# Kernel optimization log

Measured on AMD Instinct MI355X. Metric: run time of the kernel, lower is better.

The kernel has to match this reference:

```python
import jax, jax.numpy as jnp
import numpy as np

B, SEQ_LEN, N_VARS, N_MARK = 16, 96, 862, 4
D_MODEL, D_STATE, D_CONV, D_FF = 512, 16, 2, 512
DT_RANK = 32  # ceil(d_model/16)
E_LAYERS = 2
PRED_LEN = 96
EPS = 1e-5


def _layer_norm(x, w, b):
    mu = x.mean(-1, keepdims=True)
    var = ((x - mu) ** 2).mean(-1, keepdims=True)
    return (x - mu) / jnp.sqrt(var + EPS) * w + b


def _selective_scan(xc, dt, Bm, Cm, A, D):
    # xc, dt: [B,S,d]; Bm, Cm: [B,S,ds]; A: [d,ds]; D: [d]
    def step(h, inp):
        x_t, dt_t, B_t, C_t = inp  # [B,d],[B,d],[B,ds],[B,ds]
        dA = jnp.exp(dt_t[..., None] * A)                      # [B,d,ds]
        h = dA * h + (dt_t * x_t)[..., None] * B_t[:, None, :]
        return h, jnp.einsum('bds,bs->bd', h, C_t)
    h0 = jnp.zeros((xc.shape[0], A.shape[0], A.shape[1]), xc.dtype)
    xs = tuple(jnp.swapaxes(t, 0, 1) for t in (xc, dt, Bm, Cm))
    _, ys = jax.lax.scan(step, h0, xs)
    return jnp.swapaxes(ys, 0, 1) + xc * D


def _mamba(x, in_W, conv_W, conv_b, xproj_W, dt_W, dt_b, A_log, D, out_W):
    d = in_W.shape[0] // 2
    xz = x @ in_W.T                                             # [B,S,2d]
    xi, z = xz[..., :d], xz[..., d:]
    xp = jnp.pad(xi, ((0, 0), (1, 0), (0, 0)))                  # causal pad, d_conv=2
    xc = xp[:, :-1] * conv_W[:, 0] + xp[:, 1:] * conv_W[:, 1] + conv_b
    xc = jax.nn.silu(xc)
    dbc = xc @ xproj_W.T                                        # [B,S,dt_rank+2*ds]
    dtr = dbc[..., :DT_RANK]
    Bm = dbc[..., DT_RANK:DT_RANK + D_STATE]
    Cm = dbc[..., DT_RANK + D_STATE:]
    dt = jax.nn.softplus(dtr @ dt_W.T + dt_b)
    A = -jnp.exp(A_log)
    y = _selective_scan(xc, dt, Bm, Cm, A, D)
    return (y * jax.nn.silu(z)) @ out_W.T


def _forward(x_enc, x_mark_enc, emb_W, emb_b,
             mf_in_W, mf_conv_W, mf_conv_b, mf_xproj_W, mf_dt_W, mf_dt_b, mf_A_log, mf_D, mf_out_W,
             mr_in_W, mr_conv_W, mr_conv_b, mr_xproj_W, mr_dt_W, mr_dt_b, mr_A_log, mr_D, mr_out_W,
             conv1_W, conv1_b, conv2_W, conv2_b, ln1_w, ln1_b, ln2_w, ln2_b,
             enc_norm_w, enc_norm_b, proj_W, proj_b):
    # RevIN-style instance normalization over time
    means = x_enc.mean(1, keepdims=True)
    xe = x_enc - means
    stdev = jnp.sqrt(jnp.mean(xe ** 2, axis=1, keepdims=True) + EPS)  # unbiased=False
    xe = xe / stdev
    N = x_enc.shape[2]
    # inverted embedding: variates (+ time marks) are tokens, Linear over time axis
    tok = jnp.concatenate([jnp.swapaxes(xe, 1, 2), jnp.swapaxes(x_mark_enc, 1, 2)], axis=1)
    x = tok @ emb_W.T + emb_b                                   # [B, N+4, d_model]
    for l in range(E_LAYERS):
        fwd = _mamba(x, mf_in_W[l], mf_conv_W[l], mf_conv_b[l], mf_xproj_W[l],
                     mf_dt_W[l], mf_dt_b[l], mf_A_log[l], mf_D[l], mf_out_W[l])
        rev = _mamba(x[:, ::-1], mr_in_W[l], mr_conv_W[l], mr_conv_b[l], mr_xproj_W[l],
                     mr_dt_W[l], mr_dt_b[l], mr_A_log[l], mr_D[l], mr_out_W[l])[:, ::-1]
        x = x + fwd + rev
        y = x = _layer_norm(x, ln1_w[l], ln1_b[l])
        y = jax.nn.relu(y @ conv1_W[l].T + conv1_b[l])          # 1x1 conv == linear
        y = y @ conv2_W[l].T + conv2_b[l]
        x = _layer_norm(x + y, ln2_w[l], ln2_b[l])
    x = _layer_norm(x, enc_norm_w, enc_norm_b)
    dec = jnp.swapaxes(x @ proj_W.T + proj_b, 1, 2)[:, :, :N]   # [B, pred_len, N]
    dec = dec * stdev[:, 0][:, None, :] + means[:, 0][:, None, :]
    return dec


def setup_inputs() -> dict:
    key = jax.random.key(0)
    ks = iter(jax.random.split(key, 64))
    nrm = lambda shape, s=0.02: jax.random.normal(next(ks), shape, jnp.float32) * s
    inp = {
        'x_enc': jax.random.normal(next(ks), (B, SEQ_LEN, N_VARS), jnp.float32),
        'x_mark_enc': jax.random.normal(next(ks), (B, SEQ_LEN, N_MARK), jnp.float32),
        'x_dec': jnp.zeros((1, 1, 1), jnp.float32),
        'x_mark_dec': jnp.zeros((1, 1, 1), jnp.float32),
        'emb_W': nrm((D_MODEL, SEQ_LEN)),
        'emb_b': jnp.zeros((D_MODEL,), jnp.float32),
    }
    for p in ('mf', 'mr'):
        inp[p + '_in_W'] = nrm((E_LAYERS, 2 * D_MODEL, D_MODEL))
        inp[p + '_conv_W'] = nrm((E_LAYERS, D_MODEL, D_CONV), 0.1)
        inp[p + '_conv_b'] = jnp.zeros((E_LAYERS, D_MODEL), jnp.float32)
        inp[p + '_xproj_W'] = nrm((E_LAYERS, DT_RANK + 2 * D_STATE, D_MODEL))
        inp[p + '_dt_W'] = nrm((E_LAYERS, D_MODEL, DT_RANK), 0.1)
        inp[p + '_dt_b'] = nrm((E_LAYERS, D_MODEL), 0.1)
        inp[p + '_A_log'] = jnp.log(jnp.broadcast_to(
            jnp.arange(1, D_STATE + 1, dtype=jnp.float32), (E_LAYERS, D_MODEL, D_STATE)))
        inp[p + '_D'] = jnp.ones((E_LAYERS, D_MODEL), jnp.float32)
        inp[p + '_out_W'] = nrm((E_LAYERS, D_MODEL, D_MODEL))
    inp['conv1_W'] = nrm((E_LAYERS, D_FF, D_MODEL))
    inp['conv1_b'] = jnp.zeros((E_LAYERS, D_FF), jnp.float32)
    inp['conv2_W'] = nrm((E_LAYERS, D_MODEL, D_FF))
    inp['conv2_b'] = jnp.zeros((E_LAYERS, D_MODEL), jnp.float32)
    inp['ln1_w'] = jnp.ones((E_LAYERS, D_MODEL), jnp.float32)
    inp['ln1_b'] = jnp.zeros((E_LAYERS, D_MODEL), jnp.float32)
    inp['ln2_w'] = jnp.ones((E_LAYERS, D_MODEL), jnp.float32)
    inp['ln2_b'] = jnp.zeros((E_LAYERS, D_MODEL), jnp.float32)
    inp['enc_norm_w'] = jnp.ones((D_MODEL,), jnp.float32)
    inp['enc_norm_b'] = jnp.zeros((D_MODEL,), jnp.float32)
    inp['proj_W'] = nrm((PRED_LEN, D_MODEL))
    inp['proj_b'] = jnp.zeros((PRED_LEN,), jnp.float32)
    return inp


def reference(x_enc, x_mark_enc, x_dec, x_mark_dec, emb_W, emb_b,
              mf_in_W, mf_conv_W, mf_conv_b, mf_xproj_W, mf_dt_W, mf_dt_b, mf_A_log, mf_D, mf_out_W,
              mr_in_W, mr_conv_W, mr_conv_b, mr_xproj_W, mr_dt_W, mr_dt_b, mr_A_log, mr_D, mr_out_W,
              conv1_W, conv1_b, conv2_W, conv2_b, ln1_w, ln1_b, ln2_w, ln2_b,
              enc_norm_w, enc_norm_b, proj_W, proj_b):
    return _forward(x_enc, x_mark_enc, emb_W, emb_b,
                    mf_in_W, mf_conv_W, mf_conv_b, mf_xproj_W, mf_dt_W, mf_dt_b, mf_A_log, mf_D, mf_out_W,
                    mr_in_W, mr_conv_W, mr_conv_b, mr_xproj_W, mr_dt_W, mr_dt_b, mr_A_log, mr_D, mr_out_W,
                    conv1_W, conv1_b, conv2_W, conv2_b, ln1_w, ln1_b, ln2_w, ln2_b,
                    enc_norm_w, enc_norm_b, proj_W, proj_b)
```

## Files before the change

kernel.cpp:

```cpp
#include <hip/hip_runtime.h>
#include <math.h>

#define BATCH   16
#define SEQ     96
#define NVARS   862
#define NMARK   4
#define LTOK    866
#define MROWS   (BATCH*LTOK)
#define DM      512
#define DSTATE  16
#define DTRANK  32
#define DFF     512
#define PRED    96
#define EPS_F   1e-5f

#define CCH     32
#define TCH     28

typedef __attribute__((ext_vector_type(4))) float f32x4;
typedef __attribute__((ext_vector_type(8))) short bf16x8;
typedef unsigned short ushort_t;

__device__ __forceinline__ short f2bf(float f) {
    unsigned u = __builtin_bit_cast(unsigned, f);
    u += 0x7fffu + ((u >> 16) & 1u);
    return (short)(u >> 16);
}
__device__ __forceinline__ float bf2f(ushort_t u) {
    return __builtin_bit_cast(float, (unsigned)u << 16);
}

__global__ __launch_bounds__(256) void gemm_bf16(
    const ushort_t* __restrict__ A, int lda,
    const ushort_t* __restrict__ W, int ldw,
    const float* __restrict__ bias,
    const float* __restrict__ res,
    float* __restrict__ out, int ldo,
    int M, int N, int K, int rev, int act, int final_mode, int gx,
    const float* __restrict__ fstd, const float* __restrict__ fmean)
{
    __shared__ ushort_t Als[128 * 32];
    __shared__ ushort_t Bls[128 * 32];
    const int tid  = threadIdx.x;
    const int lane = tid & 63;
    const int w    = tid >> 6;
    const int wm   = w >> 1;
    const int wn   = w & 1;

    const int nwg = gridDim.x;
    const int orig = blockIdx.x;
    const int q = nwg >> 3, r = nwg & 7;
    const int xcd = orig & 7, idx = orig >> 3;
    const int swz = (xcd < r ? xcd * (q + 1) : r * (q + 1) + (xcd - r) * q) + idx;
    const int m0 = (swz / gx) * 128, n0 = (swz % gx) * 128;

    const int srow = tid >> 1;
    const int sh   = tid & 1;
    int gm = m0 + srow; if (gm > M - 1) gm = M - 1;
    int rm = gm;
    if (rev) { int b = gm / LTOK; int t = gm - b * LTOK; rm = b * LTOK + (LTOK - 1 - t); }
    const size_t aoff = (size_t)rm * lda + sh * 16;
    int gn = n0 + srow; if (gn > N - 1) gn = N - 1;
    const size_t woff = (size_t)gn * ldw + sh * 16;
    const int swz0 = ((sh * 2 + 0) ^ ((srow >> 1) & 3)) * 8;
    const int swz1 = ((sh * 2 + 1) ^ ((srow >> 1) & 3)) * 8;
    ushort_t* Awp = &Als[srow * 32];
    ushort_t* Bwp = &Bls[srow * 32];

    f32x4 acc[4][4];
#pragma unroll
    for (int i = 0; i < 4; ++i)
#pragma unroll
        for (int j = 0; j < 4; ++j) { f32x4 z = {0.f, 0.f, 0.f, 0.f}; acc[i][j] = z; }

    const int fr = lane & 15;
    const int kg = lane >> 4;
    const int cg = (kg ^ ((fr >> 1) & 3)) * 8;

    for (int k0 = 0; k0 < K; k0 += 32) {
        const bf16x8 a0 = *(const bf16x8*)(A + aoff + k0);
        const bf16x8 a1 = *(const bf16x8*)(A + aoff + k0 + 8);
        const bf16x8 b0 = *(const bf16x8*)(W + woff + k0);
        const bf16x8 b1 = *(const bf16x8*)(W + woff + k0 + 8);
        __syncthreads();
        *(bf16x8*)(Awp + swz0) = a0;
        *(bf16x8*)(Awp + swz1) = a1;
        *(bf16x8*)(Bwp + swz0) = b0;
        *(bf16x8*)(Bwp + swz1) = b1;
        __syncthreads();

        bf16x8 a4[4], b4[4];
#pragma unroll
        for (int i = 0; i < 4; ++i) {
            a4[i] = *(const bf16x8*)&Als[(wm * 64 + i * 16 + fr) * 32 + cg];
            b4[i] = *(const bf16x8*)&Bls[(wn * 64 + i * 16 + fr) * 32 + cg];
        }
#pragma unroll
        for (int mi = 0; mi < 4; ++mi)
#pragma unroll
            for (int ni = 0; ni < 4; ++ni)
                acc[mi][ni] = __builtin_amdgcn_mfma_f32_16x16x32_bf16(
                    a4[mi], b4[ni], acc[mi][ni], 0, 0, 0);
    }

#pragma unroll
    for (int mi = 0; mi < 4; ++mi) {
#pragma unroll
        for (int ni = 0; ni < 4; ++ni) {
            const int gnn = n0 + wn * 64 + ni * 16 + fr;
            if (gnn >= N) continue;
#pragma unroll
            for (int j = 0; j < 4; ++j) {
                const int gmm = m0 + wm * 64 + mi * 16 + kg * 4 + j;
                if (gmm >= M) continue;
                float v = acc[mi][ni][j];
                if (bias) v += bias[gnn];
                if (act == 1) v = fmaxf(v, 0.f);
                else if (act == 2) v = (v > 20.f) ? v : log1pf(__expf(v));
                if (res) v += res[(size_t)gmm * DM + gnn];
                if (!final_mode) {
                    out[(size_t)gmm * ldo + gnn] = v;
                } else {
                    const int bb = gmm / LTOK, vv = gmm - bb * LTOK;
                    if (vv < NVARS) {
                        out[((size_t)bb * PRED + gnn) * NVARS + vv] =
                            v * fstd[bb * NVARS + vv] + fmean[bb * NVARS + vv];
                    }
                }
            }
        }
    }
}

__global__ void cast_kernel(const float* __restrict__ src, ushort_t* __restrict__ dst, int n)
{
    for (int i = blockIdx.x * blockDim.x + threadIdx.x; i < n; i += gridDim.x * blockDim.x)
        dst[i] = (ushort_t)f2bf(src[i]);
}

struct CvtJobs {
    const float* src[12];
    ushort_t*    dst[12];
    int          n[12];
};
__global__ void cvt_kernel(CvtJobs jobs) {
    const int j = blockIdx.y;
    const float* s = jobs.src[j];
    ushort_t* d = jobs.dst[j];
    const int n = jobs.n[j];
    for (int i = blockIdx.x * blockDim.x + threadIdx.x; i < n; i += gridDim.x * blockDim.x)
        d[i] = (ushort_t)f2bf(s[i]);
}

__global__ void stats_kernel(const float* __restrict__ x_enc,
                             float* __restrict__ means, float* __restrict__ stdev)
{
    int i = blockIdx.x * blockDim.x + threadIdx.x;
    if (i >= BATCH * NVARS) return;
    int b = i / NVARS, v = i - b * NVARS;
    const float* p = x_enc + (size_t)b * SEQ * NVARS + v;
    float s = 0.f;
    for (int t = 0; t < SEQ; ++t) s += p[(size_t)t * NVARS];
    float mu = s / (float)SEQ;
    float ss = 0.f;
    for (int t = 0; t < SEQ; ++t) { float d = p[(size_t)t * NVARS] - mu; ss += d * d; }
    means[i] = mu;
    stdev[i] = sqrtf(ss / (float)SEQ + EPS_F);
}

__global__ void tok_kernel(const float* __restrict__ x_enc, const float* __restrict__ x_mark,
                           const float* __restrict__ means, const float* __restrict__ stdev,
                           ushort_t* __restrict__ tok)
{
    int i = blockIdx.x * blockDim.x + threadIdx.x;
    if (i >= MROWS * SEQ) return;
    int s = i % SEQ;
    int row = i / SEQ;
    int b = row / LTOK, l = row - b * LTOK;
    float val;
    if (l < NVARS) {
        val = (x_enc[((size_t)b * SEQ + s) * NVARS + l] - means[b * NVARS + l])
              / stdev[b * NVARS + l];
    } else {
        val = x_mark[((size_t)b * SEQ + s) * NMARK + (l - NVARS)];
    }
    tok[i] = (ushort_t)f2bf(val);
}

__global__ void conv_silu_kernel(const float* __restrict__ xz, float* __restrict__ xc,
                                 ushort_t* __restrict__ xc_bf,
                                 const float* __restrict__ cW, const float* __restrict__ cb)
{
    int i = blockIdx.x * blockDim.x + threadIdx.x;
    if (i >= MROWS * DM) return;
    int d = i & (DM - 1);
    int row = i >> 9;
    int t = row % LTOK;
    float cur = xz[(size_t)row * 1024 + d];
    float prev = (t == 0) ? 0.f : xz[(size_t)(row - 1) * 1024 + d];
    float v = prev * cW[d * 2 + 0] + cur * cW[d * 2 + 1] + cb[d];
    float sv = v * (1.f / (1.f + __expf(-v)));
    xc[i] = sv;
    xc_bf[i] = (ushort_t)f2bf(sv);
}

__global__ __launch_bounds__(256) void scan1_kernel(
    const float* __restrict__ xc, const float* __restrict__ dt,
    const float* __restrict__ dbc, const float* __restrict__ A_log,
    float* __restrict__ aprod, float* __restrict__ hpart)
{
    __shared__ float Ls[TCH * 32];
    const int tid = threadIdx.x;
    const int d = blockIdx.x * 256 + tid;
    const int c = blockIdx.y;
    const int b = blockIdx.z;
    const int t0 = c * TCH;
    const int tend = min(t0 + TCH, LTOK);
    const size_t rowb = (size_t)b * LTOK;

    for (int i = tid; i < TCH * 32; i += 256) {
        const int tr = min(t0 + (i >> 5), LTOK - 1);
        Ls[i] = dbc[(rowb + tr) * 64 + 32 + (i & 31)];
    }
    __syncthreads();

    float Ads[16];
#pragma unroll
    for (int s = 0; s < 16; ++s) Ads[s] = -__expf(A_log[d * DSTATE + s]);
    float h[16];
#pragma unroll
    for (int s = 0; s < 16; ++s) h[s] = 0.f;
    float sumdt = 0.f;

    for (int t = t0; t < tend; ++t) {
        const size_t row = rowb + t;
        const float dtv = dt[row * DM + d];
        const float xcv = xc[row * DM + d];
        const float du = dtv * xcv;
        sumdt += dtv;
        const float* Bp = &Ls[(t - t0) * 32];
#pragma unroll
        for (int s = 0; s < 16; ++s) {
            const float dA = __expf(dtv * Ads[s]);
            h[s] = dA * h[s] + du * Bp[s];
        }
    }
#pragma unroll
    for (int s = 0; s < 16; ++s) {
        const size_t oidx = ((size_t)(b * CCH + c) * 16 + s) * DM + d;
        aprod[oidx] = __expf(Ads[s] * sumdt);
        hpart[oidx] = h[s];
    }
}

__global__ __launch_bounds__(256) void scan2_kernel(
    float* __restrict__ aprod, const float* __restrict__ hpart)
{
    const int gid = blockIdx.x * 256 + threadIdx.x;
    const int d = gid & (DM - 1);
    const int s = (gid >> 9) & 15;
    const int b = gid >> 13;
    float h = 0.f;
    for (int c = 0; c < CCH; ++c) {
        const size_t idx = ((size_t)(b * CCH + c) * 16 + s) * DM + d;
        const float ap = aprod[idx];
        const float hp = hpart[idx];
        aprod[idx] = h;
        h = hp + ap * h;
    }
}

__global__ __launch_bounds__(256) void scan3_kernel(
    const float* __restrict__ xc, const float* __restrict__ dt,
    const float* __restrict__ dbc, const float* __restrict__ xz,
    const float* __restrict__ A_log, const float* __restrict__ Dp,
    const float* __restrict__ hinit, ushort_t* __restrict__ ym)
{
    __shared__ float Ls[TCH * 32];
    const int tid = threadIdx.x;
    const int d = blockIdx.x * 256 + tid;
    const int c = blockIdx.y;
    const int b = blockIdx.z;
    const int t0 = c * TCH;
    const int tend = min(t0 + TCH, LTOK);
    const size_t rowb = (size_t)b * LTOK;

    for (int i = tid; i < TCH * 32; i += 256) {
        const int tr = min(t0 + (i >> 5), LTOK - 1);
        Ls[i] = dbc[(rowb + tr) * 64 + 32 + (i & 31)];
    }
    __syncthreads();

    float Ads[16];
#pragma unroll
    for (int s = 0; s < 16; ++s) Ads[s] = -__expf(A_log[d * DSTATE + s]);
    float h[16];
#pragma unroll
    for (int s = 0; s < 16; ++s)
        h[s] = hinit[((size_t)(b * CCH + c) * 16 + s) * DM + d];
    const float Dd = Dp[d];

    for (int t = t0; t < tend; ++t) {
        const size_t row = rowb + t;
        const float dtv = dt[row * DM + d];
        const float xcv = xc[row * DM + d];
        const float du = dtv * xcv;
        const float* Bp = &Ls[(t - t0) * 32];
        float p0 = 0.f, p1 = 0.f, p2 = 0.f, p3 = 0.f;
#pragma unroll
        for (int s = 0; s < 16; ++s) {
            const float dA = __expf(dtv * Ads[s]);
            const float hn = dA * h[s] + du * Bp[s];
            h[s] = hn;
            const float pc = hn * Bp[16 + s];
            if ((s & 3) == 0) p0 += pc;
            else if ((s & 3) == 1) p1 += pc;
            else if ((s & 3) == 2) p2 += pc;
            else p3 += pc;
        }
        const float y = (p0 + p1) + (p2 + p3) + xcv * Dd;
        const float z = xz[row * 1024 + DM + d];
        ym[row * DM + d] = (ushort_t)f2bf(y * (z * (1.f / (1.f + __expf(-z)))));
    }
}

__global__ __launch_bounds__(256) void ln_kernel(const float* __restrict__ in,
                                                 const float* __restrict__ w,
                                                 const float* __restrict__ bp,
                                                 float* __restrict__ outf,
                                                 ushort_t* __restrict__ outb)
{
    const int row = blockIdx.x;
    const int tid = threadIdx.x;
    const float2 v = *(const float2*)(in + (size_t)row * DM + tid * 2);
    float s  = v.x + v.y;
    float ss = v.x * v.x + v.y * v.y;
    for (int off = 32; off; off >>= 1) {
        s  += __shfl_down(s, off);
        ss += __shfl_down(ss, off);
    }
    __shared__ float sh[10];
    const int wid = tid >> 6, lane = tid & 63;
    if (lane == 0) { sh[wid] = s; sh[4 + wid] = ss; }
    __syncthreads();
    if (tid == 0) {
        float S = sh[0] + sh[1] + sh[2] + sh[3];
        float SS = sh[4] + sh[5] + sh[6] + sh[7];
        float mu = S / (float)DM;
        float var = SS / (float)DM - mu * mu;
        sh[8] = mu; sh[9] = rsqrtf(var + EPS_F);
    }
    __syncthreads();
    const float mu = sh[8], rstd = sh[9];
    const int c = tid * 2;
    float2 o;
    o.x = (v.x - mu) * rstd * w[c]     + bp[c];
    o.y = (v.y - mu) * rstd * w[c + 1] + bp[c + 1];
    if (outf) *(float2*)(outf + (size_t)row * DM + c) = o;
    if (outb) {
        unsigned pk = (unsigned)(ushort_t)f2bf(o.x) | ((unsigned)(ushort_t)f2bf(o.y) << 16);
        ((unsigned*)outb)[(size_t)row * (DM / 2) + tid] = pk;
    }
}

static inline void launch_gemm(hipStream_t st, const ushort_t* A, int lda,
                               const ushort_t* W, int ldw, const float* bias,
                               const float* res, float* out, int ldo,
                               int M, int N, int K, int rev, int act, int fin = 0,
                               const float* fstd = nullptr, const float* fmean = nullptr)
{
    const int gx = (N + 127) / 128, gy = (M + 127) / 128;
    hipLaunchKernelGGL(gemm_bf16, dim3(gx * gy), dim3(256), 0, st,
                       A, lda, W, ldw, bias, res, out, ldo,
                       M, N, K, rev, act, fin, gx, fstd, fmean);
}

extern "C" void kernel_launch(void* const* d_in, const int* in_sizes, int n_in,
                              void* d_out, int out_size, void* d_ws, size_t ws_size,
                              hipStream_t stream)
{
    const float* x_enc   = (const float*)d_in[0];
    const float* x_mark  = (const float*)d_in[1];
    const float* emb_W   = (const float*)d_in[4];
    const float* emb_b   = (const float*)d_in[5];
    const float* m_in_W[2]    = { (const float*)d_in[6],  (const float*)d_in[15] };
    const float* m_conv_W[2]  = { (const float*)d_in[7],  (const float*)d_in[16] };
    const float* m_conv_b[2]  = { (const float*)d_in[8],  (const float*)d_in[17] };
    const float* m_xproj_W[2] = { (const float*)d_in[9],  (const float*)d_in[18] };
    const float* m_dt_W[2]    = { (const float*)d_in[10], (const float*)d_in[19] };
    const float* m_dt_b[2]    = { (const float*)d_in[11], (const float*)d_in[20] };
    const float* m_A_log[2]   = { (const float*)d_in[12], (const float*)d_in[21] };
    const float* m_D[2]       = { (const float*)d_in[13], (const float*)d_in[22] };
    const float* m_out_W[2]   = { (const float*)d_in[14], (const float*)d_in[23] };
    const float* conv1_W = (const float*)d_in[24];
    const float* conv1_b = (const float*)d_in[25];
    const float* conv2_W = (const float*)d_in[26];
    const float* conv2_b = (const float*)d_in[27];
    const float* ln1_w = (const float*)d_in[28];
    const float* ln1_b = (const float*)d_in[29];
    const float* ln2_w = (const float*)d_in[30];
    const float* ln2_b = (const float*)d_in[31];
    const float* enc_w = (const float*)d_in[32];
    const float* enc_b = (const float*)d_in[33];
    const float* proj_W = (const float*)d_in[34];
    const float* proj_b = (const float*)d_in[35];

    const size_t MD = (size_t)MROWS * DM;
    float* ws = (float*)d_ws;
    size_t o = 0;
    float* means = ws + o; o += 13824;
    float* stdev = ws + o; o += 13824;
    float* xbuf  = ws + o; o += MD;
    float* accb  = ws + o; o += MD;
    float* xzb   = ws + o; o += 2 * MD;
    float* xcb   = ws + o; o += MD;
    float* dtb   = ws + o; o += MD;
    float* dbcb  = ws + o; o += (size_t)MROWS * 64;
    float* hpart = ws + o; o += (size_t)BATCH * CCH * 16 * DM;
    float* x2f   = xzb;
    float* hbuf  = xzb + MD;

    ushort_t* wsb = (ushort_t*)(ws + o);
    size_t so = 0;
    ushort_t* xbuf_bf = wsb + so; so += MD;
    ushort_t* ybuf_bf = wsb + so; so += MD;
    ushort_t* xcb_bf  = wsb + so; so += MD;
    ushort_t* x2_bf   = wsb + so; so += MD;
    ushort_t* dbcb_bf = wsb + so; so += (size_t)MROWS * 64;
    ushort_t* embW_bf = wsb + so; so += 49152;
    ushort_t* inW_bf[2];  inW_bf[0] = wsb + so; so += 1048576; inW_bf[1] = wsb + so; so += 1048576;
    ushort_t* xpW_bf[2];  xpW_bf[0] = wsb + so; so += 65536;   xpW_bf[1] = wsb + so; so += 65536;
    ushort_t* dtW_bf[2];  dtW_bf[0] = wsb + so; so += 32768;   dtW_bf[1] = wsb + so; so += 32768;
    ushort_t* outW_bf[2]; outW_bf[0] = wsb + so; so += 524288; outW_bf[1] = wsb + so; so += 524288;
    ushort_t* c1W_bf = wsb + so; so += 524288;
    ushort_t* c2W_bf = wsb + so; so += 524288;
    ushort_t* projW_bf = wsb + so; so += 49152;
    ushort_t* tok_bf = x2_bf;
    ushort_t* hb_bf  = ybuf_bf;
    float* aprod = (float*)xcb_bf;

    CvtJobs jobs;
    jobs.src[0] = emb_W;      jobs.dst[0] = embW_bf;    jobs.n[0] = 49152;
    jobs.src[1] = m_in_W[0];  jobs.dst[1] = inW_bf[0];  jobs.n[1] = 1048576;
    jobs.src[2] = m_in_W[1];  jobs.dst[2] = inW_bf[1];  jobs.n[2] = 1048576;
    jobs.src[3] = m_xproj_W[0]; jobs.dst[3] = xpW_bf[0]; jobs.n[3] = 65536;
    jobs.src[4] = m_xproj_W[1]; jobs.dst[4] = xpW_bf[1]; jobs.n[4] = 65536;
    jobs.src[5] = m_dt_W[0];  jobs.dst[5] = dtW_bf[0];  jobs.n[5] = 32768;
    jobs.src[6] = m_dt_W[1];  jobs.dst[6] = dtW_bf[1];  jobs.n[6] = 32768;
    jobs.src[7] = m_out_W[0]; jobs.dst[7] = outW_bf[0]; jobs.n[7] = 524288;
    jobs.src[8] = m_out_W[1]; jobs.dst[8] = outW_bf[1]; jobs.n[8] = 524288;
    jobs.src[9] = conv1_W;    jobs.dst[9] = c1W_bf;     jobs.n[9] = 524288;
    jobs.src[10] = conv2_W;   jobs.dst[10] = c2W_bf;    jobs.n[10] = 524288;
    jobs.src[11] = proj_W;    jobs.dst[11] = projW_bf;  jobs.n[11] = 49152;
    hipLaunchKernelGGL(cvt_kernel, dim3(64, 12), dim3(256), 0, stream, jobs);

    hipLaunchKernelGGL(stats_kernel, dim3((BATCH * NVARS + 255) / 256), dim3(256), 0, stream,
                       x_enc, means, stdev);
    hipLaunchKernelGGL(tok_kernel, dim3((MROWS * SEQ + 255) / 256), dim3(256), 0, stream,
                       x_enc, x_mark, means, stdev, tok_bf);
    launch_gemm(stream, tok_bf, SEQ, embW_bf, SEQ, emb_b, nullptr,
                xbuf, DM, MROWS, DM, SEQ, 0, 0);
    hipLaunchKernelGGL(cast_kernel, dim3(2048), dim3(256), 0, stream,
                       xbuf, xbuf_bf, (int)MD);

    for (int l = 0; l < 2; ++l) {
        for (int dir = 0; dir < 2; ++dir) {
            const ushort_t* inW  = inW_bf[dir]  + (size_t)l * 2 * DM * DM;
            const float* cW   = m_conv_W[dir]  + (size_t)l * DM * 2;
            const float* cb   = m_conv_b[dir]  + (size_t)l * DM;
            const ushort_t* xpW  = xpW_bf[dir] + (size_t)l * 64 * DM;
            const ushort_t* dtW  = dtW_bf[dir] + (size_t)l * DM * DTRANK;
            const float* dtbias = m_dt_b[dir]  + (size_t)l * DM;
            const float* Alog = m_A_log[dir]   + (size_t)l * DM * DSTATE;
            const float* Dp   = m_D[dir]       + (size_t)l * DM;
            const ushort_t* outW = outW_bf[dir] + (size_t)l * DM * DM;

            launch_gemm(stream, xbuf_bf, DM, inW, DM, nullptr, nullptr,
                        xzb, 1024, MROWS, 2 * DM, DM, dir, 0);
            hipLaunchKernelGGL(conv_silu_kernel, dim3((MROWS * DM + 255) / 256), dim3(256),
                               0, stream, xzb, xcb, xcb_bf, cW, cb);
            launch_gemm(stream, xcb_bf, DM, xpW, DM, nullptr, nullptr,
                        dbcb, 64, MROWS, 64, DM, 0, 0);
            hipLaunchKernelGGL(cast_kernel, dim3(512), dim3(256), 0, stream,
                               dbcb, dbcb_bf, MROWS * 64);
            launch_gemm(stream, dbcb_bf, 64, dtW, DTRANK, dtbias, nullptr,
                        dtb, DM, MROWS, DM, DTRANK, 0, 2);
            hipLaunchKernelGGL(scan1_kernel, dim3(2, CCH, BATCH), dim3(256), 0, stream,
                               xcb, dtb, dbcb, Alog, aprod, hpart);
            hipLaunchKernelGGL(scan2_kernel, dim3((BATCH * 16 * DM) / 256), dim3(256), 0, stream,
                               aprod, hpart);
            hipLaunchKernelGGL(scan3_kernel, dim3(2, CCH, BATCH), dim3(256), 0, stream,
                               xcb, dtb, dbcb, xzb, Alog, Dp, aprod, ybuf_bf);
            launch_gemm(stream, ybuf_bf, DM, outW, DM, nullptr,
                        dir == 0 ? xbuf : accb,
                        accb, DM, MROWS, DM, DM, dir, 0);
        }
        hipLaunchKernelGGL(ln_kernel, dim3(MROWS), dim3(256), 0, stream,
                           accb, ln1_w + l * DM, ln1_b + l * DM, x2f, x2_bf);
        launch_gemm(stream, x2_bf, DM, c1W_bf + (size_t)l * DFF * DM, DM,
                    conv1_b + l * DFF, nullptr,
                    hbuf, DFF, MROWS, DFF, DM, 0, 1);
        hipLaunchKernelGGL(cast_kernel, dim3(2048), dim3(256), 0, stream,
                           hbuf, hb_bf, (int)MD);
        launch_gemm(stream, hb_bf, DFF, c2W_bf + (size_t)l * DM * DFF, DFF,
                    conv2_b + l * DM, x2f,
                    accb, DM, MROWS, DM, DFF, 0, 0);
        hipLaunchKernelGGL(ln_kernel, dim3(MROWS), dim3(256), 0, stream,
                           accb, ln2_w + l * DM, ln2_b + l * DM, xbuf, xbuf_bf);
    }

    hipLaunchKernelGGL(ln_kernel, dim3(MROWS), dim3(256), 0, stream,
                       xbuf, enc_w, enc_b, nullptr, x2_bf);
    launch_gemm(stream, x2_bf, DM, projW_bf, DM, proj_b, nullptr,
                (float*)d_out, 0, MROWS, PRED, DM, 0, 0, 1, stdev, means);
}
```

Measured before the change: 1.583 ms.

## Run reverse Mamba in-place and fuse both out-projections into one K=1024 GEMM

Drops the reversed-row gather in the GEMM A-load. The backward direction now runs its conv and its scan chunks in reverse time order instead. Both directions write gated outputs into one concatenated [M,1024] buffer, and a single GEMM against concatenated out-projection weights replaces two GEMMs and the accb read-modify-write. The GEMM main loop also register-prefetches the next K-tile's global loads before the MMA work. The cost is an extra weight concat-convert kernel, and hpart now aliases accb.

```diff
diff --git a/kernel.cpp b/kernel.cpp
--- a/kernel.cpp
+++ b/kernel.cpp
@@ -36,7 +36,7 @@
     const float* __restrict__ bias,
     const float* __restrict__ res,
     float* __restrict__ out, int ldo,
-    int M, int N, int K, int rev, int act, int final_mode, int gx,
+    int M, int N, int K, int act, int final_mode, int gx,
     const float* __restrict__ fstd, const float* __restrict__ fmean)
 {
     __shared__ ushort_t Als[128 * 32];
@@ -57,9 +57,7 @@
     const int srow = tid >> 1;
     const int sh   = tid & 1;
     int gm = m0 + srow; if (gm > M - 1) gm = M - 1;
-    int rm = gm;
-    if (rev) { int b = gm / LTOK; int t = gm - b * LTOK; rm = b * LTOK + (LTOK - 1 - t); }
-    const size_t aoff = (size_t)rm * lda + sh * 16;
+    const size_t aoff = (size_t)gm * lda + sh * 16;
     int gn = n0 + srow; if (gn > N - 1) gn = N - 1;
     const size_t woff = (size_t)gn * ldw + sh * 16;
     const int swz0 = ((sh * 2 + 0) ^ ((srow >> 1) & 3)) * 8;
@@ -77,17 +75,24 @@
     const int kg = lane >> 4;
     const int cg = (kg ^ ((fr >> 1) & 3)) * 8;
 
+    bf16x8 a0 = *(const bf16x8*)(A + aoff);
+    bf16x8 a1 = *(const bf16x8*)(A + aoff + 8);
+    bf16x8 b0 = *(const bf16x8*)(W + woff);
+    bf16x8 b1 = *(const bf16x8*)(W + woff + 8);
+
     for (int k0 = 0; k0 < K; k0 += 32) {
-        const bf16x8 a0 = *(const bf16x8*)(A + aoff + k0);
-        const bf16x8 a1 = *(const bf16x8*)(A + aoff + k0 + 8);
-        const bf16x8 b0 = *(const bf16x8*)(W + woff + k0);
-        const bf16x8 b1 = *(const bf16x8*)(W + woff + k0 + 8);
         __syncthreads();
         *(bf16x8*)(Awp + swz0) = a0;
         *(bf16x8*)(Awp + swz1) = a1;
         *(bf16x8*)(Bwp + swz0) = b0;
         *(bf16x8*)(Bwp + swz1) = b1;
         __syncthreads();
+
+        const int kn = (k0 + 32 < K) ? (k0 + 32) : k0;
+        a0 = *(const bf16x8*)(A + aoff + kn);
+        a1 = *(const bf16x8*)(A + aoff + kn + 8);
+        b0 = *(const bf16x8*)(W + woff + kn);
+        b1 = *(const bf16x8*)(W + woff + kn + 8);
 
         bf16x8 a4[4], b4[4];
 #pragma unroll
@@ -138,6 +143,16 @@
         dst[i] = (ushort_t)f2bf(src[i]);
 }
 
+__global__ void cvtcat_kernel(const float* __restrict__ fa, const float* __restrict__ fb,
+                              ushort_t* __restrict__ dst, int n_elems)
+{
+    int i = blockIdx.x * blockDim.x + threadIdx.x;
+    if (i >= n_elems) return;
+    int n = i >> 10, k = i & 1023;
+    float v = (k < 512) ? fa[n * 512 + k] : fb[n * 512 + (k - 512)];
+    dst[i] = (ushort_t)f2bf(v);
+}
+
 struct CvtJobs {
     const float* src[12];
     ushort_t*    dst[12];
@@ -189,7 +204,8 @@
 
 __global__ void conv_silu_kernel(const float* __restrict__ xz, float* __restrict__ xc,
                                  ushort_t* __restrict__ xc_bf,
-                                 const float* __restrict__ cW, const float* __restrict__ cb)
+                                 const float* __restrict__ cW, const float* __restrict__ cb,
+                                 int dir)
 {
     int i = blockIdx.x * blockDim.x + threadIdx.x;
     if (i >= MROWS * DM) return;
@@ -197,8 +213,10 @@
     int row = i >> 9;
     int t = row % LTOK;
     float cur = xz[(size_t)row * 1024 + d];
-    float prev = (t == 0) ? 0.f : xz[(size_t)(row - 1) * 1024 + d];
-    float v = prev * cW[d * 2 + 0] + cur * cW[d * 2 + 1] + cb[d];
+    float oth;
+    if (dir == 0) oth = (t == 0)        ? 0.f : xz[(size_t)(row - 1) * 1024 + d];
+    else          oth = (t == LTOK - 1) ? 0.f : xz[(size_t)(row + 1) * 1024 + d];
+    float v = oth * cW[d * 2 + 0] + cur * cW[d * 2 + 1] + cb[d];
     float sv = v * (1.f / (1.f + __expf(-v)));
     xc[i] = sv;
     xc_bf[i] = (ushort_t)f2bf(sv);
@@ -207,7 +225,7 @@
 __global__ __launch_bounds__(256) void scan1_kernel(
     const float* __restrict__ xc, const float* __restrict__ dt,
     const float* __restrict__ dbc, const float* __restrict__ A_log,
-    float* __restrict__ aprod, float* __restrict__ hpart)
+    float* __restrict__ aprod, float* __restrict__ hpart, int dir)
 {
     __shared__ float Ls[TCH * 32];
     const int tid = threadIdx.x;
@@ -232,7 +250,9 @@
     for (int s = 0; s < 16; ++s) h[s] = 0.f;
     float sumdt = 0.f;
 
-    for (int t = t0; t < tend; ++t) {
+    int t = dir ? tend - 1 : t0;
+    const int step = dir ? -1 : 1;
+    for (int it = 0; it < tend - t0; ++it, t += step) {
         const size_t row = rowb + t;
         const float dtv = dt[row * DM + d];
         const float xcv = xc[row * DM + d];
@@ -254,18 +274,19 @@
 }
 
 __global__ __launch_bounds__(256) void scan2_kernel(
-    float* __restrict__ aprod, const float* __restrict__ hpart)
+    float* __restrict__ aprod, const float* __restrict__ hpart, int dir)
 {
     const int gid = blockIdx.x * 256 + threadIdx.x;
     const int d = gid & (DM - 1);
     const int s = (gid >> 9) & 15;
     const int b = gid >> 13;
     float h = 0.f;
-    for (int c = 0; c < CCH; ++c) {
-        const size_t idx = ((size_t)(b * CCH + c) * 16 + s) * DM + d;
-        const float ap = aprod[idx];
-        const float hp = hpart[idx];
-        aprod[idx] = h;
+    for (int ci = 0; ci < CCH; ++ci) {
+        const int c = dir ? (CCH - 1 - ci) : ci;
+        const size_t idxc = ((size_t)(b * CCH + c) * 16 + s) * DM + d;
+        const float ap = aprod[idxc];
+        const float hp = hpart[idxc];
+        aprod[idxc] = h;
         h = hp + ap * h;
     }
 }
@@ -274,7 +295,7 @@
     const float* __restrict__ xc, const float* __restrict__ dt,
     const float* __restrict__ dbc, const float* __restrict__ xz,
     const float* __restrict__ A_log, const float* __restrict__ Dp,
-    const float* __restrict__ hinit, ushort_t* __restrict__ ym)
+    const float* __restrict__ hinit, ushort_t* __restrict__ ymcat, int dir)
 {
     __shared__ float Ls[TCH * 32];
     const int tid = threadIdx.x;
@@ -300,7 +321,9 @@
         h[s] = hinit[((size_t)(b * CCH + c) * 16 + s) * DM + d];
     const float Dd = Dp[d];
 
-    for (int t = t0; t < tend; ++t) {
+    int t = dir ? tend - 1 : t0;
+    const int step = dir ? -1 : 1;
+    for (int it = 0; it < tend - t0; ++it, t += step) {
         const size_t row = rowb + t;
         const float dtv = dt[row * DM + d];
         const float xcv = xc[row * DM + d];
@@ -320,7 +343,8 @@
         }
         const float y = (p0 + p1) + (p2 + p3) + xcv * Dd;
         const float z = xz[row * 1024 + DM + d];
-        ym[row * DM + d] = (ushort_t)f2bf(y * (z * (1.f / (1.f + __expf(-z)))));
+        ymcat[row * 1024 + dir * DM + d] =
+            (ushort_t)f2bf(y * (z * (1.f / (1.f + __expf(-z)))));
     }
 }
 
@@ -366,13 +390,13 @@
 static inline void launch_gemm(hipStream_t st, const ushort_t* A, int lda,
                                const ushort_t* W, int ldw, const float* bias,
                                const float* res, float* out, int ldo,
-                               int M, int N, int K, int rev, int act, int fin = 0,
+                               int M, int N, int K, int act, int fin = 0,
                                const float* fstd = nullptr, const float* fmean = nullptr)
 {
     const int gx = (N + 127) / 128, gy = (M + 127) / 128;
     hipLaunchKernelGGL(gemm_bf16, dim3(gx * gy), dim3(256), 0, st,
                        A, lda, W, ldw, bias, res, out, ldo,
-                       M, N, K, rev, act, fin, gx, fstd, fmean);
+                       M, N, K, act, fin, gx, fstd, fmean);
 }
 
 extern "C" void kernel_launch(void* const* d_in, const int* in_sizes, int n_in,
@@ -416,14 +440,13 @@
     float* xcb   = ws + o; o += MD;
     float* dtb   = ws + o; o += MD;
     float* dbcb  = ws + o; o += (size_t)MROWS * 64;
-    float* hpart = ws + o; o += (size_t)BATCH * CCH * 16 * DM;
     float* x2f   = xzb;
     float* hbuf  = xzb + MD;
 
     ushort_t* wsb = (ushort_t*)(ws + o);
     size_t so = 0;
     ushort_t* xbuf_bf = wsb + so; so += MD;
-    ushort_t* ybuf_bf = wsb + so; so += MD;
+    ushort_t* ymcat   = wsb + so; so += 2 * MD;
     ushort_t* xcb_bf  = wsb + so; so += MD;
     ushort_t* x2_bf   = wsb + so; so += MD;
     ushort_t* dbcb_bf = wsb + so; so += (size_t)MROWS * 64;
@@ -431,35 +454,41 @@
     ushort_t* inW_bf[2];  inW_bf[0] = wsb + so; so += 1048576; inW_bf[1] = wsb + so; so += 1048576;
     ushort_t* xpW_bf[2];  xpW_bf[0] = wsb + so; so += 65536;   xpW_bf[1] = wsb + so; so += 65536;
     ushort_t* dtW_bf[2];  dtW_bf[0] = wsb + so; so += 32768;   dtW_bf[1] = wsb + so; so += 32768;
-    ushort_t* outW_bf[2]; outW_bf[0] = wsb + so; so += 524288; outW_bf[1] = wsb + so; so += 524288;
+    ushort_t* outWcat[2]; outWcat[0] = wsb + so; so += 524288; outWcat[1] = wsb + so; so += 524288;
     ushort_t* c1W_bf = wsb + so; so += 524288;
     ushort_t* c2W_bf = wsb + so; so += 524288;
     ushort_t* projW_bf = wsb + so; so += 49152;
     ushort_t* tok_bf = x2_bf;
-    ushort_t* hb_bf  = ybuf_bf;
+    ushort_t* hb_bf  = ymcat;
     float* aprod = (float*)xcb_bf;
+    float* hpart = accb;
 
     CvtJobs jobs;
-    jobs.src[0] = emb_W;      jobs.dst[0] = embW_bf;    jobs.n[0] = 49152;
-    jobs.src[1] = m_in_W[0];  jobs.dst[1] = inW_bf[0];  jobs.n[1] = 1048576;
-    jobs.src[2] = m_in_W[1];  jobs.dst[2] = inW_bf[1];  jobs.n[2] = 1048576;
+    jobs.src[0] = emb_W;        jobs.dst[0] = embW_bf;   jobs.n[0] = 49152;
+    jobs.src[1] = m_in_W[0];    jobs.dst[1] = inW_bf[0]; jobs.n[1] = 1048576;
+    jobs.src[2] = m_in_W[1];    jobs.dst[2] = inW_bf[1]; jobs.n[2] = 1048576;
     jobs.src[3] = m_xproj_W[0]; jobs.dst[3] = xpW_bf[0]; jobs.n[3] = 65536;
     jobs.src[4] = m_xproj_W[1]; jobs.dst[4] = xpW_bf[1]; jobs.n[4] = 65536;
-    jobs.src[5] = m_dt_W[0];  jobs.dst[5] = dtW_bf[0];  jobs.n[5] = 32768;
-    jobs.src[6] = m_dt_W[1];  jobs.dst[6] = dtW_bf[1];  jobs.n[6] = 32768;
-    jobs.src[7] = m_out_W[0]; jobs.dst[7] = outW_bf[0]; jobs.n[7] = 524288;
-    jobs.src[8] = m_out_W[1]; jobs.dst[8] = outW_bf[1]; jobs.n[8] = 524288;
-    jobs.src[9] = conv1_W;    jobs.dst[9] = c1W_bf;     jobs.n[9] = 524288;
-    jobs.src[10] = conv2_W;   jobs.dst[10] = c2W_bf;    jobs.n[10] = 524288;
-    jobs.src[11] = proj_W;    jobs.dst[11] = projW_bf;  jobs.n[11] = 49152;
+    jobs.src[5] = m_dt_W[0];    jobs.dst[5] = dtW_bf[0]; jobs.n[5] = 32768;
+    jobs.src[6] = m_dt_W[1];    jobs.dst[6] = dtW_bf[1]; jobs.n[6] = 32768;
+    jobs.src[7] = conv1_W;      jobs.dst[7] = c1W_bf;    jobs.n[7] = 524288;
+    jobs.src[8] = conv2_W;      jobs.dst[8] = c2W_bf;    jobs.n[8] = 524288;
+    jobs.src[9] = proj_W;       jobs.dst[9] = projW_bf;  jobs.n[9] = 49152;
+    jobs.src[10] = emb_W;       jobs.dst[10] = embW_bf;  jobs.n[10] = 0;
+    jobs.src[11] = emb_W;       jobs.dst[11] = embW_bf;  jobs.n[11] = 0;
     hipLaunchKernelGGL(cvt_kernel, dim3(64, 12), dim3(256), 0, stream, jobs);
+    for (int l = 0; l < 2; ++l)
+        hipLaunchKernelGGL(cvtcat_kernel, dim3((512 * 1024 + 255) / 256), dim3(256), 0, stream,
+                           m_out_W[0] + (size_t)l * DM * DM,
+                           m_out_W[1] + (size_t)l * DM * DM,
+                           outWcat[l], 512 * 1024);
 
     hipLaunchKernelGGL(stats_kernel, dim3((BATCH * NVARS + 255) / 256), dim3(256), 0, stream,
                        x_enc, means, stdev);
     hipLaunchKernelGGL(tok_kernel, dim3((MROWS * SEQ + 255) / 256), dim3(256), 0, stream,
                        x_enc, x_mark, means, stdev, tok_bf);
     launch_gemm(stream, tok_bf, SEQ, embW_bf, SEQ, emb_b, nullptr,
-                xbuf, DM, MROWS, DM, SEQ, 0, 0);
+                xbuf, DM, MROWS, DM, SEQ, 0);
     hipLaunchKernelGGL(cast_kernel, dim3(2048), dim3(256), 0, stream,
                        xbuf, xbuf_bf, (int)MD);
 
@@ -473,38 +502,36 @@
             const float* dtbias = m_dt_b[dir]  + (size_t)l * DM;
             const float* Alog = m_A_log[dir]   + (size_t)l * DM * DSTATE;
             const float* Dp   = m_D[dir]       + (size_t)l * DM;
-            const ushort_t* outW = outW_bf[dir] + (size_t)l * DM * DM;
 
             launch_gemm(stream, xbuf_bf, DM, inW, DM, nullptr, nullptr,
-                        xzb, 1024, MROWS, 2 * DM, DM, dir, 0);
+                        xzb, 1024, MROWS, 2 * DM, DM, 0);
             hipLaunchKernelGGL(conv_silu_kernel, dim3((MROWS * DM + 255) / 256), dim3(256),
-                               0, stream, xzb, xcb, xcb_bf, cW, cb);
+                               0, stream, xzb, xcb, xcb_bf, cW, cb, dir);
             launch_gemm(stream, xcb_bf, DM, xpW, DM, nullptr, nullptr,
-                        dbcb, 64, MROWS, 64, DM, 0, 0);
+                        dbcb, 64, MROWS, 64, DM, 0);
             hipLaunchKernelGGL(cast_kernel, dim3(512), dim3(256), 0, stream,
                                dbcb, dbcb_bf, MROWS * 64);
             launch_gemm(stream, dbcb_bf, 64, dtW, DTRANK, dtbias, nullptr,
-                        dtb, DM, MROWS, DM, DTRANK, 0, 2);
+                        dtb, DM, MROWS, DM, DTRANK, 2);
             hipLaunchKernelGGL(scan1_kernel, dim3(2, CCH, BATCH), dim3(256), 0, stream,
-                               xcb, dtb, dbcb, Alog, aprod, hpart);
+                               xcb, dtb, dbcb, Alog, aprod, hpart, dir);
             hipLaunchKernelGGL(scan2_kernel, dim3((BATCH * 16 * DM) / 256), dim3(256), 0, stream,
-                               aprod, hpart);
+                               aprod, hpart, dir);
             hipLaunchKernelGGL(scan3_kernel, dim3(2, CCH, BATCH), dim3(256), 0, stream,
-                               xcb, dtb, dbcb, xzb, Alog, Dp, aprod, ybuf_bf);
-            launch_gemm(stream, ybuf_bf, DM, outW, DM, nullptr,
-                        dir == 0 ? xbuf : accb,
-                        accb, DM, MROWS, DM, DM, dir, 0);
+                               xcb, dtb, dbcb, xzb, Alog, Dp, aprod, ymcat, dir);
         }
+        launch_gemm(stream, ymcat, 1024, outWcat[l], 1024, nullptr,
+                    xbuf, accb, DM, MROWS, DM, 1024, 0);
         hipLaunchKernelGGL(ln_kernel, dim3(MROWS), dim3(256), 0, stream,
                            accb, ln1_w + l * DM, ln1_b + l * DM, x2f, x2_bf);
         launch_gemm(stream, x2_bf, DM, c1W_bf + (size_t)l * DFF * DM, DM,
                     conv1_b + l * DFF, nullptr,
-                    hbuf, DFF, MROWS, DFF, DM, 0, 1);
+                    hbuf, DFF, MROWS, DFF, DM, 1);
         hipLaunchKernelGGL(cast_kernel, dim3(2048), dim3(256), 0, stream,
                            hbuf, hb_bf, (int)MD);
         launch_gemm(stream, hb_bf, DFF, c2W_bf + (size_t)l * DM * DFF, DFF,
                     conv2_b + l * DM, x2f,
-                    accb, DM, MROWS, DM, DFF, 0, 0);
+                    accb, DM, MROWS, DM, DFF, 0);
         hipLaunchKernelGGL(ln_kernel, dim3(MROWS), dim3(256), 0, stream,
                            accb, ln2_w + l * DM, ln2_b + l * DM, xbuf, xbuf_bf);
     }
@@ -512,5 +539,5 @@
     hipLaunchKernelGGL(ln_kernel, dim3(MROWS), dim3(256), 0, stream,
                        xbuf, enc_w, enc_b, nullptr, x2_bf);
     launch_gemm(stream, x2_bf, DM, projW_bf, DM, proj_b, nullptr,
-                (float*)d_out, 0, MROWS, PRED, DM, 0, 0, 1, stdev, means);
-}
+                (float*)d_out, 0, MROWS, PRED, DM, 0, 1, stdev, means);
+}
```

New measurement: 1.718 ms. 8.6% more time.
